# Performance work log

Hardware: AMD Instinct MI355X
Metric: run time of the kernel (lower is better)

The kernel has to match this reference:

```python
import jax, jax.numpy as jnp
import numpy as np

B, L, H = 2, 64, 64
VOCAB = 32000
HEADS = 8
HPH = H // HEADS  # harmonics per head


def setup_inputs() -> dict:
    key = jax.random.key(0)
    ks = jax.random.split(key, 6)
    freqs = jax.random.normal(ks[0], (B, L, H), dtype=jnp.float32)
    amps = jax.random.normal(ks[1], (B, L, H), dtype=jnp.float32)
    phases = jax.random.normal(ks[2], (B, L, H), dtype=jnp.float32)
    vocab_patterns = jax.random.normal(ks[3], (VOCAB, HEADS, HPH), dtype=jnp.float32)
    # nn.Parameter init is zeros; use small noise so gradients/paths are nontrivial
    interference_phases = 0.1 * jax.random.normal(ks[4], (HEADS, HPH), dtype=jnp.float32)
    # nn.Linear(num_heads, 1): weight (1, heads), bias (1,)
    W = jax.random.normal(ks[5], (1, HEADS), dtype=jnp.float32) / np.sqrt(HEADS)
    b = jnp.zeros((1,), dtype=jnp.float32)
    return {"freqs": freqs, "amps": amps, "phases": phases,
            "vocab_patterns": vocab_patterns,
            "interference_phases": interference_phases,
            "W": W, "b": b}


def reference(freqs, amps, phases, vocab_patterns, interference_phases, W, b):
    Bb, Ll, Hh = freqs.shape
    heads = vocab_patterns.shape[1]
    hph = Hh // heads
    f = freqs.reshape(Bb, Ll, heads, hph)
    a = amps.reshape(Bb, Ll, heads, hph)
    p = phases.reshape(Bb, Ll, heads, hph)
    # phase_alignment has no vocab dependence: fold amp * cos(phase diff) first
    c = a * jnp.cos(p - interference_phases[None, None, :, :])  # (B,L,heads,hph)
    scores = []
    for h in range(heads):  # small fixed loop over heads (avoids (B,L,heads,V,hph) blowup)
        f_h = f[:, :, h, :]                      # (B,L,hph)
        vf = vocab_patterns[:, h, :]             # (V,hph)
        fm = jnp.exp(-jnp.abs(f_h[:, :, None, :] - vf[None, None, :, :]))  # (B,L,V,hph)
        scores.append(jnp.einsum('blk,blvk->blv', c[:, :, h, :], fm))
    s = jnp.stack(scores, axis=-1)               # (B,L,V,heads)
    logits = jnp.einsum('blvh,oh->blvo', s, W)[..., 0] + b[0]  # (B,L,V)
    return logits
```

## Files before the change

kernel.cpp:

```cpp
#include <hip/hip_runtime.h>
#include <math.h>

#define VOCAB   32000
#define BLTOT   128
#define HTOT    64
#define BLT     4
#define VPB     256
#define VT      2
#define NSLICE  ((VOCAB + VPB * VT - 1) / (VPB * VT))

#define LOG2E   1.44269504088896340736f

typedef __fp16 h2 __attribute__((ext_vector_type(2)));

__global__ void prep_kernel(const float* __restrict__ freqs,
                            const float* __restrict__ amps,
                            const float* __restrict__ phases,
                            const float* __restrict__ ip,
                            const float* __restrict__ W,
                            void* __restrict__ ws) {
    int t = blockIdx.x * blockDim.x + threadIdx.x;
    if (t >= BLTOT * HTOT) return;
    int bl = t >> 6;
    int j  = t & 63;
    float fe = freqs[t] * LOG2E;
    float cw = amps[t] * cosf(phases[t] - ip[j]) * W[j >> 3];
    int jj = j >> 2, u = j & 3;
    __fp16* pA = (__fp16*)ws;
    __fp16* pC = (__fp16*)((char*)ws + 32768);
    int ia = (bl * 16 + jj) * 8;
    pA[ia + u]     = (__fp16)__builtin_amdgcn_exp2f(fe);
    pA[ia + 4 + u] = (__fp16)__builtin_amdgcn_exp2f(-fe);
    pC[(bl * 16 + jj) * 4 + u] = (__fp16)cw;
}

__global__ __launch_bounds__(VPB, 8) void
wave_main(const float4* __restrict__ vp4,
          const void* __restrict__ uni,
          const float* __restrict__ bptr,
          float* __restrict__ out) {
    const int tid = threadIdx.x;
    const int bl0 = blockIdx.x * BLT;
    const int v0  = blockIdx.y * (VPB * VT) + tid;

    __shared__ float4 smemA[BLT * 16];
    __shared__ float2 smemC[BLT * 16];

    {
        const float4* gA = (const float4*)((const char*)uni + (size_t)bl0 * 256);
        const float2* gC = (const float2*)((const char*)uni + 32768 + (size_t)bl0 * 128);
        if (tid < BLT * 16)            smemA[tid]            = gA[tid];
        else if (tid < 2 * BLT * 16)   smemC[tid - BLT * 16] = gC[tid - BLT * 16];
    }
    __syncthreads();

    int vidx[VT];
#pragma unroll
    for (int k = 0; k < VT; ++k) {
        int v = v0 + k * VPB;
        vidx[k] = v < VOCAB ? v : VOCAB - 1;
    }

    float acc[BLT][VT];
#pragma unroll
    for (int i = 0; i < BLT; ++i)
#pragma unroll
        for (int k = 0; k < VT; ++k) acc[i][k] = 0.0f;

#pragma unroll 2
    for (int jj = 0; jj < 16; ++jj) {
        h2 evA[VT], evB[VT], emvA[VT], emvB[VT];
#pragma unroll
        for (int k = 0; k < VT; ++k) {
            const float4 vf = vp4[vidx[k] * 16 + jj];
            float ax = vf.x * LOG2E, ay = vf.y * LOG2E;
            float az = vf.z * LOG2E, aw = vf.w * LOG2E;
            evA[k]  = __builtin_amdgcn_cvt_pkrtz(__builtin_amdgcn_exp2f( ax),
                                                 __builtin_amdgcn_exp2f( ay));
            evB[k]  = __builtin_amdgcn_cvt_pkrtz(__builtin_amdgcn_exp2f( az),
                                                 __builtin_amdgcn_exp2f( aw));
            emvA[k] = __builtin_amdgcn_cvt_pkrtz(__builtin_amdgcn_exp2f(-ax),
                                                 __builtin_amdgcn_exp2f(-ay));
            emvB[k] = __builtin_amdgcn_cvt_pkrtz(__builtin_amdgcn_exp2f(-az),
                                                 __builtin_amdgcn_exp2f(-aw));
        }
#pragma unroll
        for (int i = 0; i < BLT; ++i) {
            const float4 A = smemA[i * 16 + jj];
            const float2 C = smemC[i * 16 + jj];
            const h2 ef01 = __builtin_bit_cast(h2, A.x);
            const h2 ef23 = __builtin_bit_cast(h2, A.y);
            const h2 em01 = __builtin_bit_cast(h2, A.z);
            const h2 em23 = __builtin_bit_cast(h2, A.w);
            const h2 cw01 = __builtin_bit_cast(h2, C.x);
            const h2 cw23 = __builtin_bit_cast(h2, C.y);
#pragma unroll
            for (int k = 0; k < VT; ++k) {
                h2 m01 = __builtin_elementwise_min(ef01 * emvA[k], em01 * evA[k]);
                h2 m23 = __builtin_elementwise_min(ef23 * emvB[k], em23 * evB[k]);
                acc[i][k] = __builtin_amdgcn_fdot2(m01, cw01, acc[i][k], false);
                acc[i][k] = __builtin_amdgcn_fdot2(m23, cw23, acc[i][k], false);
            }
        }
    }

    const float b0 = bptr[0];
#pragma unroll
    for (int i = 0; i < BLT; ++i)
#pragma unroll
        for (int k = 0; k < VT; ++k) {
            int v = v0 + k * VPB;
            if (v < VOCAB)
                out[(bl0 + i) * VOCAB + v] = acc[i][k] + b0;
        }
}

extern "C" void kernel_launch(void* const* d_in, const int* in_sizes, int n_in,
                              void* d_out, int out_size, void* d_ws, size_t ws_size,
                              hipStream_t stream) {
    const float* freqs  = (const float*)d_in[0];
    const float* amps   = (const float*)d_in[1];
    const float* phases = (const float*)d_in[2];
    const float* vp     = (const float*)d_in[3];
    const float* ip     = (const float*)d_in[4];
    const float* W      = (const float*)d_in[5];
    const float* b      = (const float*)d_in[6];
    float* out = (float*)d_out;

    prep_kernel<<<dim3(32), dim3(256), 0, stream>>>(freqs, amps, phases, ip, W, d_ws);

    wave_main<<<dim3(BLTOT / BLT, NSLICE), dim3(VPB), 0, stream>>>(
        (const float4*)vp, d_ws, b, out);
}
```

Before: 115.6 us.

## Precompute vocab exponentials in a separate kernel with coalesced transposed layout

Adds a prep kernel that evaluates exp(±vocab_pattern) once per vocab entry and stores them as packed fp16 in a jj-major layout, so the main kernel loads precomputed values with coalesced reads. Before this, every (bl-block, vocab) block recomputed the 8 exp2 calls per float4, 32 times over, and read the vocab patterns with a stride. VT also grows from 2 to 4, giving more vocab items per thread. The cost is an extra launch and 8 MB of workspace traffic, plus higher register pressure from the larger VT.

Result: no change. 115.3 us (-0.3%).

```diff
diff --git a/kernel.cpp b/kernel.cpp
--- a/kernel.cpp
+++ b/kernel.cpp
@@ -6,8 +6,9 @@
 #define HTOT    64
 #define BLT     4
 #define VPB     256
-#define VT      2
-#define NSLICE  ((VOCAB + VPB * VT - 1) / (VPB * VT))
+#define VT      4
+#define SLICE   (VPB * VT)
+#define NSLICE  ((VOCAB + SLICE - 1) / SLICE)
 
 #define LOG2E   1.44269504088896340736f
 
@@ -34,18 +35,42 @@
     pC[(bl * 16 + jj) * 4 + u] = (__fp16)cw;
 }
 
+__global__ void prep_exp_kernel(const float4* __restrict__ vp4,
+                                float4* __restrict__ evt4) {
+    int t = blockIdx.x * blockDim.x + threadIdx.x;
+    if (t >= VOCAB * 16) return;
+    int jj = t / VOCAB;
+    int v  = t - jj * VOCAB;
+    const float4 vf = vp4[v * 16 + jj];
+    float ax = vf.x * LOG2E, ay = vf.y * LOG2E;
+    float az = vf.z * LOG2E, aw = vf.w * LOG2E;
+    h2 ev01  = __builtin_amdgcn_cvt_pkrtz(__builtin_amdgcn_exp2f( ax),
+                                          __builtin_amdgcn_exp2f( ay));
+    h2 ev23  = __builtin_amdgcn_cvt_pkrtz(__builtin_amdgcn_exp2f( az),
+                                          __builtin_amdgcn_exp2f( aw));
+    h2 emv01 = __builtin_amdgcn_cvt_pkrtz(__builtin_amdgcn_exp2f(-ax),
+                                          __builtin_amdgcn_exp2f(-ay));
+    h2 emv23 = __builtin_amdgcn_cvt_pkrtz(__builtin_amdgcn_exp2f(-az),
+                                          __builtin_amdgcn_exp2f(-aw));
+    float4 o;
+    o.x = __builtin_bit_cast(float, ev01);
+    o.y = __builtin_bit_cast(float, ev23);
+    o.z = __builtin_bit_cast(float, emv01);
+    o.w = __builtin_bit_cast(float, emv23);
+    evt4[t] = o;
+}
+
 __global__ __launch_bounds__(VPB, 8) void
-wave_main(const float4* __restrict__ vp4,
+wave_main(const float4* __restrict__ evt4,
           const void* __restrict__ uni,
           const float* __restrict__ bptr,
           float* __restrict__ out) {
     const int tid = threadIdx.x;
     const int bl0 = blockIdx.x * BLT;
-    const int v0  = blockIdx.y * (VPB * VT) + tid;
+    const int v0  = blockIdx.y * SLICE + tid;
 
     __shared__ float4 smemA[BLT * 16];
     __shared__ float2 smemC[BLT * 16];
-
     {
         const float4* gA = (const float4*)((const char*)uni + (size_t)bl0 * 256);
         const float2* gC = (const float2*)((const char*)uni + 32768 + (size_t)bl0 * 128);
@@ -72,17 +97,11 @@
         h2 evA[VT], evB[VT], emvA[VT], emvB[VT];
 #pragma unroll
         for (int k = 0; k < VT; ++k) {
-            const float4 vf = vp4[vidx[k] * 16 + jj];
-            float ax = vf.x * LOG2E, ay = vf.y * LOG2E;
-            float az = vf.z * LOG2E, aw = vf.w * LOG2E;
-            evA[k]  = __builtin_amdgcn_cvt_pkrtz(__builtin_amdgcn_exp2f( ax),
-                                                 __builtin_amdgcn_exp2f( ay));
-            evB[k]  = __builtin_amdgcn_cvt_pkrtz(__builtin_amdgcn_exp2f( az),
-                                                 __builtin_amdgcn_exp2f( aw));
-            emvA[k] = __builtin_amdgcn_cvt_pkrtz(__builtin_amdgcn_exp2f(-ax),
-                                                 __builtin_amdgcn_exp2f(-ay));
-            emvB[k] = __builtin_amdgcn_cvt_pkrtz(__builtin_amdgcn_exp2f(-az),
-                                                 __builtin_amdgcn_exp2f(-aw));
+            const float4 E = evt4[jj * VOCAB + vidx[k]];
+            evA[k]  = __builtin_bit_cast(h2, E.x);
+            evB[k]  = __builtin_bit_cast(h2, E.y);
+            emvA[k] = __builtin_bit_cast(h2, E.z);
+            emvB[k] = __builtin_bit_cast(h2, E.w);
         }
 #pragma unroll
         for (int i = 0; i < BLT; ++i) {
@@ -129,6 +148,10 @@
 
     prep_kernel<<<dim3(32), dim3(256), 0, stream>>>(freqs, amps, phases, ip, W, d_ws);
 
+    float4* evt4 = (float4*)((char*)d_ws + 49152);
+    prep_exp_kernel<<<dim3((VOCAB * 16 + 255) / 256), dim3(256), 0, stream>>>(
+        (const float4*)vp, evt4);
+
     wave_main<<<dim3(BLTOT / BLT, NSLICE), dim3(VPB), 0, stream>>>(
-        (const float4*)vp, d_ws, b, out);
+        evt4, d_ws, b, out);
 }
```
